# Kernel tuning notes

Hardware: AMD Instinct MI355X
Metric: run time of the kernel (lower is better)

The kernel has to match this reference:

```python
import jax, jax.numpy as jnp
import numpy as np

IN_DIM, HID, MEM, OUT = 512, 1024, 1024, 512
BATCH = 4096
HIST = 5  # hist_steps hard-coded in MMU.__init__

_LINEARS = [("inpgate", IN_DIM, HID), ("rec_inpgate", OUT, HID), ("mem_inpgate", MEM, HID),
            ("inp", IN_DIM, HID), ("rec_inp", OUT, HID),
            ("readgate", IN_DIM, MEM), ("rec_readgate", OUT, MEM), ("mem_readgate", MEM, MEM),
            ("decoder", HID, MEM),
            ("writegate", IN_DIM, MEM), ("rec_writegate", OUT, MEM), ("mem_writegate", MEM, MEM),
            ("encoder", MEM, HID)]


def setup_inputs() -> dict:
    key = jax.random.key(0)
    ks = iter(jax.random.split(key, 2 * len(_LINEARS) + 4))
    d = {"input": jax.random.normal(next(ks), (IN_DIM, BATCH), jnp.float32)}
    for name, fin, fout in _LINEARS:
        bound = 1.0 / np.sqrt(fin)  # torch nn.Linear default init range
        d["W_" + name] = jax.random.uniform(next(ks), (fout, fin), jnp.float32, -bound, bound)
        d["b_" + name] = jax.random.uniform(next(ks), (fout,), jnp.float32, -bound, bound)
    d["w_hid_out"] = jax.random.uniform(next(ks), (OUT, MEM), jnp.float32)  # torch.rand
    return d


def reference(input, W_inpgate, b_inpgate, W_rec_inpgate, b_rec_inpgate,
              W_mem_inpgate, b_mem_inpgate, W_inp, b_inp, W_rec_inp, b_rec_inp,
              W_readgate, b_readgate, W_rec_readgate, b_rec_readgate,
              W_mem_readgate, b_mem_readgate, W_decoder, b_decoder,
              W_writegate, b_writegate, W_rec_writegate, b_rec_writegate,
              W_mem_writegate, b_mem_writegate, W_encoder, b_encoder, w_hid_out):
    B = input.shape[1]
    lin = lambda x, W, b: x @ W.T + b
    # fresh module: history is zeros except last slot = current input (transposed to [B, in])
    xs = jnp.concatenate([jnp.zeros((HIST - 1, B, IN_DIM), input.dtype), input.T[None]], axis=0)

    def step(carry, x):
        out, mem = carry  # [B, OUT], [B, MEM]
        block_inp = jax.nn.sigmoid(lin(x, W_inp, b_inp) + lin(out, W_rec_inp, b_rec_inp))
        inp_gate = jax.nn.sigmoid(lin(x, W_inpgate, b_inpgate) + lin(mem, W_mem_inpgate, b_mem_inpgate)
                                  + lin(out, W_rec_inpgate, b_rec_inpgate))
        read_gate = jax.nn.sigmoid(lin(x, W_readgate, b_readgate) + lin(mem, W_mem_readgate, b_mem_readgate)
                                   + lin(out, W_rec_readgate, b_rec_readgate))
        decoded_mem = lin(read_gate * mem, W_decoder, b_decoder)
        hidden = decoded_mem + block_inp * inp_gate  # [B, HID] (HID == MEM)
        write_gate = jax.nn.sigmoid(lin(x, W_writegate, b_writegate) + lin(mem, W_mem_writegate, b_mem_writegate)
                                    + lin(out, W_rec_writegate, b_rec_writegate))
        encoded = jnp.tanh(lin(hidden, W_encoder, b_encoder))
        mem = (1.0 - write_gate) * mem + write_gate * encoded
        out = hidden @ w_hid_out.T  # w_hid_out.mm(hidden.T).T
        return (out, mem), None

    init = (jnp.zeros((B, OUT), input.dtype), jnp.zeros((B, MEM), input.dtype))
    (out, _mem), _ = jax.lax.scan(step, init, xs)
    return out
```

## Files before the change

kernel.cpp:

```cpp
#include <hip/hip_runtime.h>
#include <hip/hip_bf16.h>
#include <math.h>

typedef __hip_bfloat16 bf16;
typedef __attribute__((ext_vector_type(8))) short s16x8;
typedef __attribute__((ext_vector_type(4))) float f32x4;

__device__ __forceinline__ float fsig(float x) {
  return __builtin_amdgcn_rcpf(1.0f + __expf(-x));
}
__device__ __forceinline__ float ftanh(float x) { return 2.0f * fsig(2.0f * x) - 1.0f; }
__device__ __forceinline__ float dot4(float4 a, float4 b) {
  return a.x * b.x + a.y * b.y + a.z * b.z + a.w * b.w;
}

__global__ void setup(const float* __restrict__ W_inp, const float* __restrict__ W_ig,
                      const float* __restrict__ W_rg, const float* __restrict__ W_ho,
                      const float* __restrict__ W_dec, const float* __restrict__ input,
                      const float* __restrict__ b_inp, const float* __restrict__ b_rinp,
                      const float* __restrict__ b_ig, const float* __restrict__ b_mig,
                      const float* __restrict__ b_rig, const float* __restrict__ b_wg,
                      const float* __restrict__ b_mwg, const float* __restrict__ b_rwg,
                      const float* __restrict__ b_dec, bf16* __restrict__ Wcat,
                      bf16* __restrict__ WhoB, bf16* __restrict__ Wcat2, bf16* __restrict__ Wdt,
                      bf16* __restrict__ Xb, float* __restrict__ out_s, float* __restrict__ mem_s,
                      float* __restrict__ hidv, float* __restrict__ wgv,
                      float* __restrict__ vout) {
  __shared__ float t[32][33];
  const int id = blockIdx.x, tid = threadIdx.x;
  if (id < 8198) {
    const int i = id * 256 + tid;
    if (i < 524288) {
      Wcat[i] = __float2bfloat16(W_inp[i]);
    } else if (i < 1048576) {
      Wcat[i] = __float2bfloat16(W_ig[i - 524288]);
    } else if (i < 1572864) {
      Wcat[i] = __float2bfloat16(W_rg[i - 1048576]);
    } else if (i < 2097152) {
      const int k = i - 1572864;
      const bf16 vv = __float2bfloat16(W_ho[k]);
      WhoB[k] = vv;
      Wcat2[(size_t)(k >> 10) * 2048 + (k & 1023)] = vv;
    } else if (i < 2098688) {
      const int tt = i - 2097152;
      if (tt < 512) out_s[tt] = 0.0f;
      else mem_s[tt - 512] = 0.0f;
    }
  } else if (id < 10246) {
    const int b = id - 8198;
    const int i0 = (b >> 7) * 32, b0 = (b & 127) * 32;
    const int tx = tid & 31, ty = tid >> 5;
#pragma unroll
    for (int r = ty; r < 32; r += 8) t[r][tx] = input[(size_t)(i0 + r) * 4096 + b0 + tx];
    __syncthreads();
#pragma unroll
    for (int r = ty; r < 32; r += 8)
      Xb[(size_t)(b0 + r) * 512 + i0 + tx] = __float2bfloat16(t[tx][r]);
  } else if (id < 11270) {
    const int b = id - 10246;
    const int j0 = (b >> 5) * 32, k0 = (b & 31) * 32;
    const int tx = tid & 31, ty = tid >> 5;
#pragma unroll
    for (int r = ty; r < 32; r += 8) t[r][tx] = W_dec[(size_t)(j0 + r) * 1024 + k0 + tx];
    __syncthreads();
#pragma unroll
    for (int r = ty; r < 32; r += 8)
      Wdt[(size_t)(k0 + r) * 1024 + j0 + tx] = __float2bfloat16(t[tx][r]);
  } else if (id < 11274) {
    const int j = (id - 11270) * 256 + tid;
    const float bi = fsig(b_inp[j] + b_rinp[j]);
    const float ig = fsig(b_ig[j] + b_mig[j] + b_rig[j]);
    hidv[j] = b_dec[j] + bi * ig;
    wgv[j] = fsig(b_wg[j] + b_mwg[j] + b_rwg[j]);
  } else {
    const int o = id - 11274;
    const float4 a = *(const float4*)(W_ho + (size_t)o * 1024 + tid * 4);
    const float4 b = *(const float4*)(b_dec + tid * 4);
    float s = dot4(a, b);
#pragma unroll
    for (int off = 32; off > 0; off >>= 1) s += __shfl_down(s, off, 64);
    if ((tid & 63) == 0) t[0][tid >> 6] = s;
    __syncthreads();
    if (tid == 0) vout[o] = t[0][0] + t[0][1] + t[0][2] + t[0][3];
  }
}

__global__ void step_gates(const float* __restrict__ Wri, const float* __restrict__ Wmig,
                           const float* __restrict__ Wrig, const float* __restrict__ Wmrg,
                           const float* __restrict__ Wrrg, const float* __restrict__ Wmwg,
                           const float* __restrict__ Wrwg, const float* __restrict__ b_inp,
                           const float* __restrict__ b_rinp, const float* __restrict__ b_ig,
                           const float* __restrict__ b_mig, const float* __restrict__ b_rig,
                           const float* __restrict__ b_rg, const float* __restrict__ b_mrg,
                           const float* __restrict__ b_rrg, const float* __restrict__ b_wg,
                           const float* __restrict__ b_mwg, const float* __restrict__ b_rwg,
                           const float* __restrict__ out_s, const float* __restrict__ mem_s,
                           float* __restrict__ rgm, float* __restrict__ h0v,
                           float* __restrict__ wgv) {
  __shared__ float red[7][4];
  const int j = blockIdx.x, tid = threadIdx.x, lane = tid & 63, wave = tid >> 6;
  const float4 z = make_float4(0.f, 0.f, 0.f, 0.f);
  const float4 o4 = (tid < 128) ? *(const float4*)(out_s + tid * 4) : z;
  const float4 m4 = *(const float4*)(mem_s + tid * 4);
  float p[7];
  p[0] = dot4((tid < 128) ? *(const float4*)(Wri + (size_t)j * 512 + tid * 4) : z, o4);
  p[1] = dot4(*(const float4*)(Wmig + (size_t)j * 1024 + tid * 4), m4);
  p[2] = dot4((tid < 128) ? *(const float4*)(Wrig + (size_t)j * 512 + tid * 4) : z, o4);
  p[3] = dot4(*(const float4*)(Wmrg + (size_t)j * 1024 + tid * 4), m4);
  p[4] = dot4((tid < 128) ? *(const float4*)(Wrrg + (size_t)j * 512 + tid * 4) : z, o4);
  p[5] = dot4(*(const float4*)(Wmwg + (size_t)j * 1024 + tid * 4), m4);
  p[6] = dot4((tid < 128) ? *(const float4*)(Wrwg + (size_t)j * 512 + tid * 4) : z, o4);
#pragma unroll
  for (int d = 0; d < 7; ++d) {
    float s = p[d];
#pragma unroll
    for (int off = 32; off > 0; off >>= 1) s += __shfl_down(s, off, 64);
    if (lane == 0) red[d][wave] = s;
  }
  __syncthreads();
  if (tid == 0) {
    float D[7];
#pragma unroll
    for (int d = 0; d < 7; ++d) D[d] = red[d][0] + red[d][1] + red[d][2] + red[d][3];
    const float abi = b_inp[j] + b_rinp[j] + D[0];
    const float aig = b_ig[j] + b_mig[j] + b_rig[j] + D[1] + D[2];
    const float arg = b_rg[j] + b_mrg[j] + b_rrg[j] + D[3] + D[4];
    const float awg = b_wg[j] + b_mwg[j] + b_rwg[j] + D[5] + D[6];
    rgm[j] = fsig(arg) * mem_s[j];
    h0v[j] = fsig(abi) * fsig(aig);
    wgv[j] = fsig(awg);
  }
}

__global__ void step_decode(const float* __restrict__ Wdec, const float* __restrict__ b_dec,
                            const float* __restrict__ rgm, const float* __restrict__ h0v,
                            float* __restrict__ hidv) {
  __shared__ float red[4];
  const int j = blockIdx.x, tid = threadIdx.x;
  const float4 a = *(const float4*)(Wdec + (size_t)j * 1024 + tid * 4);
  const float4 b = *(const float4*)(rgm + tid * 4);
  float s = dot4(a, b);
#pragma unroll
  for (int off = 32; off > 0; off >>= 1) s += __shfl_down(s, off, 64);
  if ((tid & 63) == 0) red[tid >> 6] = s;
  __syncthreads();
  if (tid == 0) hidv[j] = b_dec[j] + red[0] + red[1] + red[2] + red[3] + h0v[j];
}

__global__ void step_update(const float* __restrict__ Wenc, const float* __restrict__ b_enc,
                            const float* __restrict__ Who, const float* __restrict__ hidv,
                            const float* __restrict__ wgv, float* __restrict__ mem_s,
                            float* __restrict__ out_s) {
  __shared__ float red[4];
  const int id = blockIdx.x, tid = threadIdx.x;
  const float* row = (id < 1024) ? (Wenc + (size_t)id * 1024) : (Who + (size_t)(id - 1024) * 1024);
  const float4 a = *(const float4*)(row + tid * 4);
  const float4 b = *(const float4*)(hidv + tid * 4);
  float s = dot4(a, b);
#pragma unroll
  for (int off = 32; off > 0; off >>= 1) s += __shfl_down(s, off, 64);
  if ((tid & 63) == 0) red[tid >> 6] = s;
  __syncthreads();
  if (tid == 0) {
    const float d = red[0] + red[1] + red[2] + red[3];
    if (id < 1024) {
      const float wg = wgv[id];
      mem_s[id] = (1.0f - wg) * mem_s[id] + wg * ftanh(b_enc[id] + d);
    } else {
      out_s[id - 1024] = d;
    }
  }
}

__global__ __launch_bounds__(256) void update0_p(
    const float* __restrict__ Wenc, const float* __restrict__ b_enc,
    const float* __restrict__ Who, const float* __restrict__ hidv,
    const float* __restrict__ wgv, float* __restrict__ mem_s, float* __restrict__ out_s,
    const bf16* __restrict__ WhoB, const bf16* __restrict__ Wdt, float* __restrict__ P) {
  __shared__ char smem[16384];
  const int tid = threadIdx.x;
  if (blockIdx.x < 1536) {
    float* red = (float*)smem;
    const int id = blockIdx.x;
    const float* row =
        (id < 1024) ? (Wenc + (size_t)id * 1024) : (Who + (size_t)(id - 1024) * 1024);
    const float4 a = *(const float4*)(row + tid * 4);
    const float4 b = *(const float4*)(hidv + tid * 4);
    float s = dot4(a, b);
#pragma unroll
    for (int off = 32; off > 0; off >>= 1) s += __shfl_down(s, off, 64);
    if ((tid & 63) == 0) red[tid >> 6] = s;
    __syncthreads();
    if (tid == 0) {
      const float d = red[0] + red[1] + red[2] + red[3];
      if (id < 1024) {
        const float wg = wgv[id];
        mem_s[id] = (1.0f - wg) * mem_s[id] + wg * ftanh(b_enc[id] + d);
      } else {
        out_s[id - 1024] = d;
      }
    }
    return;
  }
  const int bi = blockIdx.x - 1536;
  const int wave = tid >> 6, lane = tid & 63;
  const int wm = wave >> 1, wn = wave & 1;
  const int m0 = ((bi >> 4) & 7) * 64, n0 = (bi & 15) * 64;
  const int kt0 = (bi >> 7) * 512;
  f32x4 acc[2][2] = {};
  for (int kt = kt0; kt < kt0 + 512; kt += 64) {
    __syncthreads();
#pragma unroll
    for (int i = 0; i < 2; ++i) {
      const int ci = i * 256 + tid;
      const int row = ci >> 3, ck = (ci & 7) ^ (row & 7);
      const bf16* g = WhoB + (size_t)(m0 + row) * 1024 + kt + ck * 8;
      const unsigned lofs = (unsigned)__builtin_amdgcn_readfirstlane((i * 256 + wave * 64) * 16);
      __builtin_amdgcn_global_load_lds(
          (const __attribute__((address_space(1))) void*)g,
          (__attribute__((address_space(3))) void*)(smem + lofs), 16, 0, 0);
    }
#pragma unroll
    for (int i = 0; i < 2; ++i) {
      const int ci = i * 256 + tid;
      const int row = ci >> 3, ck = (ci & 7) ^ (row & 7);
      const bf16* g = Wdt + (size_t)(n0 + row) * 1024 + kt + ck * 8;
      const unsigned lofs =
          (unsigned)__builtin_amdgcn_readfirstlane(8192 + (i * 256 + wave * 64) * 16);
      __builtin_amdgcn_global_load_lds(
          (const __attribute__((address_space(1))) void*)g,
          (__attribute__((address_space(3))) void*)(smem + lofs), 16, 0, 0);
    }
    __syncthreads();
#pragma unroll
    for (int ks = 0; ks < 2; ++ks) {
      const int ckk = ks * 4 + (lane >> 4);
      s16x8 af[2];
#pragma unroll
      for (int i = 0; i < 2; ++i) {
        const int R = wm * 32 + i * 16 + (lane & 15);
        af[i] = *(const s16x8*)(smem + (R * 8 + (ckk ^ (R & 7))) * 16);
      }
#pragma unroll
      for (int j = 0; j < 2; ++j) {
        const int R = wn * 32 + j * 16 + (lane & 15);
        const s16x8 bfr = *(const s16x8*)(smem + 8192 + (R * 8 + (ckk ^ (R & 7))) * 16);
#pragma unroll
        for (int i = 0; i < 2; ++i)
          acc[i][j] = __builtin_amdgcn_mfma_f32_16x16x32_bf16(af[i], bfr, acc[i][j], 0, 0, 0);
      }
    }
  }
  const int mb = (lane >> 4) * 4, nb = lane & 15;
#pragma unroll
  for (int i = 0; i < 2; ++i) {
#pragma unroll
    for (int j = 0; j < 2; ++j) {
      const int col = n0 + wn * 32 + j * 16 + nb;
#pragma unroll
      for (int r = 0; r < 4; ++r) {
        const int rowg = m0 + wm * 32 + i * 16 + mb + r;
        atomicAdd(P + (size_t)rowg * 1024 + col, acc[i][j][r]);
      }
    }
  }
}

__global__ void final_consts(const float* __restrict__ Wri, const float* __restrict__ Wmig,
                             const float* __restrict__ Wrig, const float* __restrict__ Wmrg,
                             const float* __restrict__ Wrrg, const float* __restrict__ b_inp,
                             const float* __restrict__ b_rinp, const float* __restrict__ b_ig,
                             const float* __restrict__ b_mig, const float* __restrict__ b_rig,
                             const float* __restrict__ b_rg, const float* __restrict__ b_mrg,
                             const float* __restrict__ b_rrg, const float* __restrict__ out_s,
                             const float* __restrict__ mem_s, const float* __restrict__ P,
                             float* __restrict__ ccat, bf16* __restrict__ Wcat2) {
  __shared__ float red[5][4];
  const int id = blockIdx.x, tid = threadIdx.x, lane = tid & 63, wave = tid >> 6;
  if (id < 1024) {
    const float4 z = make_float4(0.f, 0.f, 0.f, 0.f);
    const float4 o4 = (tid < 128) ? *(const float4*)(out_s + tid * 4) : z;
    const float4 m4 = *(const float4*)(mem_s + tid * 4);
    float p[5];
    p[0] = dot4((tid < 128) ? *(const float4*)(Wri + (size_t)id * 512 + tid * 4) : z, o4);
    p[1] = dot4(*(const float4*)(Wmig + (size_t)id * 1024 + tid * 4), m4);
    p[2] = dot4((tid < 128) ? *(const float4*)(Wrig + (size_t)id * 512 + tid * 4) : z, o4);
    p[3] = dot4(*(const float4*)(Wmrg + (size_t)id * 1024 + tid * 4), m4);
    p[4] = dot4((tid < 128) ? *(const float4*)(Wrrg + (size_t)id * 512 + tid * 4) : z, o4);
#pragma unroll
    for (int d = 0; d < 5; ++d) {
      float s = p[d];
#pragma unroll
      for (int off = 32; off > 0; off >>= 1) s += __shfl_down(s, off, 64);
      if (lane == 0) red[d][wave] = s;
    }
    __syncthreads();
    if (tid == 0) {
      float D[5];
#pragma unroll
      for (int d = 0; d < 5; ++d) D[d] = red[d][0] + red[d][1] + red[d][2] + red[d][3];
      ccat[id] = b_inp[id] + b_rinp[id] + D[0];
      ccat[1024 + id] = b_ig[id] + b_mig[id] + b_rig[id] + D[1] + D[2];
      ccat[2048 + id] = b_rg[id] + b_mrg[id] + b_rrg[id] + D[3] + D[4];
    }
  } else {
    const int idx = (id - 1024) * 256 + tid;
    const int q = idx >> 10, k = idx & 1023;
    Wcat2[(size_t)q * 2048 + 1024 + k] = __float2bfloat16(P[idx] * mem_s[k]);
  }
}

__global__ __launch_bounds__(256, 4) void gemm_gates(const bf16* __restrict__ A,
                                                     const bf16* __restrict__ Wcat,
                                                     const float* __restrict__ ccat,
                                                     bf16* __restrict__ Hcat) {
  __shared__ char smem[32768];
  const int tid = threadIdx.x, wave = tid >> 6, lane = tid & 63;
  const int wm = wave >> 1, wn = wave & 1;
  const int m0 = blockIdx.y * 64, n0 = blockIdx.x * 64;
  f32x4 acc[3][2][2] = {};

  for (int kt = 0; kt < 512; kt += 64) {
    __syncthreads();
#pragma unroll
    for (int i = 0; i < 2; ++i) {
      const int ci = i * 256 + tid;
      const int row = ci >> 3, ck = (ci & 7) ^ (row & 7);
      const bf16* g = A + (size_t)(m0 + row) * 512 + kt + ck * 8;
      const unsigned lofs = (unsigned)__builtin_amdgcn_readfirstlane((i * 256 + wave * 64) * 16);
      __builtin_amdgcn_global_load_lds(
          (const __attribute__((address_space(1))) void*)g,
          (__attribute__((address_space(3))) void*)(smem + lofs), 16, 0, 0);
    }
#pragma unroll
    for (int gI = 0; gI < 3; ++gI) {
      const bf16* Bp = Wcat + gI * 524288;
#pragma unroll
      for (int i = 0; i < 2; ++i) {
        const int ci = i * 256 + tid;
        const int row = ci >> 3, ck = (ci & 7) ^ (row & 7);
        const bf16* g = Bp + (size_t)(n0 + row) * 512 + kt + ck * 8;
        const unsigned lofs = (unsigned)__builtin_amdgcn_readfirstlane(
            8192 + gI * 8192 + (i * 256 + wave * 64) * 16);
        __builtin_amdgcn_global_load_lds(
            (const __attribute__((address_space(1))) void*)g,
            (__attribute__((address_space(3))) void*)(smem + lofs), 16, 0, 0);
      }
    }
    __syncthreads();

#pragma unroll
    for (int ks = 0; ks < 2; ++ks) {
      const int ckk = ks * 4 + (lane >> 4);
      s16x8 af[2];
#pragma unroll
      for (int i = 0; i < 2; ++i) {
        const int R = wm * 32 + i * 16 + (lane & 15);
        af[i] = *(const s16x8*)(smem + (R * 8 + (ckk ^ (R & 7))) * 16);
      }
#pragma unroll
      for (int gI = 0; gI < 3; ++gI) {
#pragma unroll
        for (int j = 0; j < 2; ++j) {
          const int R = wn * 32 + j * 16 + (lane & 15);
          const s16x8 bfr =
              *(const s16x8*)(smem + 8192 + gI * 8192 + (R * 8 + (ckk ^ (R & 7))) * 16);
#pragma unroll
          for (int i = 0; i < 2; ++i)
            acc[gI][i][j] =
                __builtin_amdgcn_mfma_f32_16x16x32_bf16(af[i], bfr, acc[gI][i][j], 0, 0, 0);
        }
      }
    }
  }

  __syncthreads();
  bf16* sm = (bf16*)smem;
  bf16* sr = (bf16*)smem + 5120;
  const int mb = (lane >> 4) * 4, nb = lane & 15;
#pragma unroll
  for (int i = 0; i < 2; ++i) {
#pragma unroll
    for (int j = 0; j < 2; ++j) {
      const int colL = wn * 32 + j * 16 + nb;
      const int jg = n0 + colL;
      const float c0 = ccat[jg], c1 = ccat[1024 + jg], c2 = ccat[2048 + jg];
#pragma unroll
      for (int r = 0; r < 4; ++r) {
        const int rowL = wm * 32 + i * 16 + mb + r;
        const float h = fsig(acc[0][i][j][r] + c0) * fsig(acc[1][i][j][r] + c1);
        const float rg = fsig(acc[2][i][j][r] + c2);
        sm[rowL * 80 + colL] = __float2bfloat16(h);
        sr[rowL * 80 + colL] = __float2bfloat16(rg);
      }
    }
  }
  __syncthreads();
#pragma unroll
  for (int pp = 0; pp < 2; ++pp) {
    const int c = pp * 256 + tid;
    const int row = c >> 3, cc = c & 7;
    const s16x8 v0 = *(const s16x8*)(sm + row * 80 + cc * 8);
    const s16x8 v1 = *(const s16x8*)(sr + row * 80 + cc * 8);
    *(s16x8*)(Hcat + (size_t)(m0 + row) * 2048 + n0 + cc * 8) = v0;
    *(s16x8*)(Hcat + (size_t)(m0 + row) * 2048 + 1024 + n0 + cc * 8) = v1;
  }
}

__global__ __launch_bounds__(256, 4) void gemm_out(const bf16* __restrict__ A,
                                                   const bf16* __restrict__ Bp,
                                                   const float* __restrict__ vout,
                                                   float* __restrict__ outF) {
  __shared__ char smem[16384];
  const int tid = threadIdx.x, wave = tid >> 6, lane = tid & 63;
  const int wm = wave >> 1, wn = wave & 1;
  const int m0 = blockIdx.y * 64, n0 = blockIdx.x * 64;
  f32x4 acc[2][2] = {};

  for (int kt = 0; kt < 2048; kt += 64) {
    __syncthreads();
#pragma unroll
    for (int i = 0; i < 2; ++i) {
      const int ci = i * 256 + tid;
      const int row = ci >> 3, ck = (ci & 7) ^ (row & 7);
      const bf16* g = A + (size_t)(m0 + row) * 2048 + kt + ck * 8;
      const unsigned lofs = (unsigned)__builtin_amdgcn_readfirstlane((i * 256 + wave * 64) * 16);
      __builtin_amdgcn_global_load_lds(
          (const __attribute__((address_space(1))) void*)g,
          (__attribute__((address_space(3))) void*)(smem + lofs), 16, 0, 0);
    }
#pragma unroll
    for (int i = 0; i < 2; ++i) {
      const int ci = i * 256 + tid;
      const int row = ci >> 3, ck = (ci & 7) ^ (row & 7);
      const bf16* g = Bp + (size_t)(n0 + row) * 2048 + kt + ck * 8;
      const unsigned lofs =
          (unsigned)__builtin_amdgcn_readfirstlane(8192 + (i * 256 + wave * 64) * 16);
      __builtin_amdgcn_global_load_lds(
          (const __attribute__((address_space(1))) void*)g,
          (__attribute__((address_space(3))) void*)(smem + lofs), 16, 0, 0);
    }
    __syncthreads();

#pragma unroll
    for (int ks = 0; ks < 2; ++ks) {
      const int ckk = ks * 4 + (lane >> 4);
      s16x8 af[2];
#pragma unroll
      for (int i = 0; i < 2; ++i) {
        const int R = wm * 32 + i * 16 + (lane & 15);
        af[i] = *(const s16x8*)(smem + (R * 8 + (ckk ^ (R & 7))) * 16);
      }
#pragma unroll
      for (int j = 0; j < 2; ++j) {
        const int R = wn * 32 + j * 16 + (lane & 15);
        const s16x8 bfr = *(const s16x8*)(smem + 8192 + (R * 8 + (ckk ^ (R & 7))) * 16);
#pragma unroll
        for (int i = 0; i < 2; ++i)
          acc[i][j] = __builtin_amdgcn_mfma_f32_16x16x32_bf16(af[i], bfr, acc[i][j], 0, 0, 0);
      }
    }
  }

  const int mb = (lane >> 4) * 4, nb = lane & 15;
#pragma unroll
  for (int i = 0; i < 2; ++i) {
#pragma unroll
    for (int j = 0; j < 2; ++j) {
      const int col = n0 + wn * 32 + j * 16 + nb;
#pragma unroll
      for (int r = 0; r < 4; ++r) {
        const int rowg = m0 + wm * 32 + i * 16 + mb + r;
        outF[(size_t)rowg * 512 + col] = acc[i][j][r] + vout[col];
      }
    }
  }
}

extern "C" void kernel_launch(void* const* d_in, const int* in_sizes, int n_in, void* d_out,
                              int out_size, void* d_ws, size_t ws_size, hipStream_t stream) {
  const float* input  = (const float*)d_in[0];
  const float* W_ig   = (const float*)d_in[1];  const float* b_ig   = (const float*)d_in[2];
  const float* W_rig  = (const float*)d_in[3];  const float* b_rig  = (const float*)d_in[4];
  const float* W_mig  = (const float*)d_in[5];  const float* b_mig  = (const float*)d_in[6];
  const float* W_inp  = (const float*)d_in[7];  const float* b_inp  = (const float*)d_in[8];
  const float* W_rinp = (const float*)d_in[9];  const float* b_rinp = (const float*)d_in[10];
  const float* W_rg   = (const float*)d_in[11]; const float* b_rg   = (const float*)d_in[12];
  const float* W_rrg  = (const float*)d_in[13]; const float* b_rrg  = (const float*)d_in[14];
  const float* W_mrg  = (const float*)d_in[15]; const float* b_mrg  = (const float*)d_in[16];
  const float* W_dec  = (const float*)d_in[17]; const float* b_dec  = (const float*)d_in[18];
  const float* W_wg   = (const float*)d_in[19]; const float* b_wg   = (const float*)d_in[20];
  const float* W_rwg  = (const float*)d_in[21]; const float* b_rwg  = (const float*)d_in[22];
  const float* W_mwg  = (const float*)d_in[23]; const float* b_mwg  = (const float*)d_in[24];
  const float* W_enc  = (const float*)d_in[25]; const float* b_enc  = (const float*)d_in[26];
  const float* W_ho   = (const float*)d_in[27];
  (void)W_wg; (void)W_rwg; (void)W_mwg;

  char* ws = (char*)d_ws;
  float* out_s = (float*)(ws + 0);
  float* mem_s = (float*)(ws + 4096);
  float* rgm   = (float*)(ws + 8192);
  float* h0v   = (float*)(ws + 12288);
  float* wgv   = (float*)(ws + 16384);
  float* hidv  = (float*)(ws + 20480);
  float* ccat  = (float*)(ws + 24576);
  float* vout  = (float*)(ws + 40960);
  float* P     = (float*)(ws + 65536);
  bf16* Xb     = (bf16*)(ws + 2162688);
  bf16* Wcat   = (bf16*)(ws + 6356992);
  bf16* WhoB   = (bf16*)(ws + 9502720);
  bf16* Wcat2  = (bf16*)(ws + 10551296);
  bf16* Wdt    = (bf16*)(ws + 12648448);
  bf16* Hcat   = (bf16*)(ws + 14745600);

  setup<<<11786, 256, 0, stream>>>(W_inp, W_ig, W_rg, W_ho, W_dec, input, b_inp, b_rinp, b_ig,
                                   b_mig, b_rig, b_wg, b_mwg, b_rwg, b_dec, Wcat, WhoB, Wcat2,
                                   Wdt, Xb, out_s, mem_s, hidv, wgv, vout);

  update0_p<<<1792, 256, 0, stream>>>(W_enc, b_enc, W_ho, hidv, wgv, mem_s, out_s, WhoB, Wdt, P);

  for (int s = 0; s < 3; ++s) {
    step_gates<<<1024, 256, 0, stream>>>(W_rinp, W_mig, W_rig, W_mrg, W_rrg, W_mwg, W_rwg, b_inp,
                                         b_rinp, b_ig, b_mig, b_rig, b_rg, b_mrg, b_rrg, b_wg,
                                         b_mwg, b_rwg, out_s, mem_s, rgm, h0v, wgv);
    step_decode<<<1024, 256, 0, stream>>>(W_dec, b_dec, rgm, h0v, hidv);
    step_update<<<1536, 256, 0, stream>>>(W_enc, b_enc, W_ho, hidv, wgv, mem_s, out_s);
  }

  final_consts<<<3072, 256, 0, stream>>>(W_rinp, W_mig, W_rig, W_mrg, W_rrg, b_inp, b_rinp, b_ig,
                                         b_mig, b_rig, b_rg, b_mrg, b_rrg, out_s, mem_s, P, ccat,
                                         Wcat2);

  gemm_gates<<<dim3(16, 64), 256, 0, stream>>>(Xb, Wcat, ccat, Hcat);

  gemm_out<<<dim3(8, 64), 256, 0, stream>>>(Hcat, Wcat2, vout, (float*)d_out);
}
```

Before: 227.7 us.

## Fold decoder into encoder via precomputed W_enc·W_dec product, drop decode kernel

Precomputes E = W_enc·W_dec (bf16 MFMA, split-K atomics) and venc = W_enc·b_dec, so each recurrent step computes the encoder and output projections directly from h0 and read_gate*mem. This removes the step_decode launch and its dependent pass over W_dec in each of the three steps. In exchange, setup does more conversion work, a 1024x1024 GEMM is added up front, and E is held at bf16-derived precision, which may shift numerics slightly.

```diff
diff --git a/kernel.cpp b/kernel.cpp
--- a/kernel.cpp
+++ b/kernel.cpp
@@ -16,16 +16,18 @@
 
 __global__ void setup(const float* __restrict__ W_inp, const float* __restrict__ W_ig,
                       const float* __restrict__ W_rg, const float* __restrict__ W_ho,
-                      const float* __restrict__ W_dec, const float* __restrict__ input,
+                      const float* __restrict__ W_dec, const float* __restrict__ W_enc,
+                      const float* __restrict__ input,
                       const float* __restrict__ b_inp, const float* __restrict__ b_rinp,
                       const float* __restrict__ b_ig, const float* __restrict__ b_mig,
                       const float* __restrict__ b_rig, const float* __restrict__ b_wg,
                       const float* __restrict__ b_mwg, const float* __restrict__ b_rwg,
                       const float* __restrict__ b_dec, bf16* __restrict__ Wcat,
                       bf16* __restrict__ WhoB, bf16* __restrict__ Wcat2, bf16* __restrict__ Wdt,
-                      bf16* __restrict__ Xb, float* __restrict__ out_s, float* __restrict__ mem_s,
+                      bf16* __restrict__ WencB, bf16* __restrict__ Xb,
+                      float* __restrict__ out_s, float* __restrict__ mem_s,
                       float* __restrict__ hidv, float* __restrict__ wgv,
-                      float* __restrict__ vout) {
+                      float* __restrict__ vout, float* __restrict__ venc) {
   __shared__ float t[32][33];
   const int id = blockIdx.x, tid = threadIdx.x;
   if (id < 8198) {
@@ -72,16 +74,128 @@
     const float ig = fsig(b_ig[j] + b_mig[j] + b_rig[j]);
     hidv[j] = b_dec[j] + bi * ig;
     wgv[j] = fsig(b_wg[j] + b_mwg[j] + b_rwg[j]);
-  } else {
-    const int o = id - 11274;
-    const float4 a = *(const float4*)(W_ho + (size_t)o * 1024 + tid * 4);
+  } else if (id < 12810) {
+    const int isv = (id < 11786);
+    const int o = isv ? (id - 11274) : (id - 11786);
+    const float* row = isv ? (W_ho + (size_t)o * 1024) : (W_enc + (size_t)o * 1024);
+    const float4 a = *(const float4*)(row + tid * 4);
     const float4 b = *(const float4*)(b_dec + tid * 4);
     float s = dot4(a, b);
 #pragma unroll
     for (int off = 32; off > 0; off >>= 1) s += __shfl_down(s, off, 64);
     if ((tid & 63) == 0) t[0][tid >> 6] = s;
     __syncthreads();
-    if (tid == 0) vout[o] = t[0][0] + t[0][1] + t[0][2] + t[0][3];
+    if (tid == 0) {
+      const float v = t[0][0] + t[0][1] + t[0][2] + t[0][3];
+      if (isv) vout[o] = v; else venc[o] = v;
+    }
+  } else {
+    const int i = (id - 12810) * 256 + tid;
+    WencB[i] = __float2bfloat16(W_enc[i]);
+  }
+}
+
+__global__ __launch_bounds__(256) void update0_pe(
+    const float* __restrict__ Wenc, const float* __restrict__ b_enc,
+    const float* __restrict__ Who, const float* __restrict__ hidv,
+    const float* __restrict__ wgv, float* __restrict__ mem_s, float* __restrict__ out_s,
+    const bf16* __restrict__ WhoB, const bf16* __restrict__ WencB,
+    const bf16* __restrict__ Wdt, float* __restrict__ P, float* __restrict__ E) {
+  __shared__ char smem[16384];
+  const int tid = threadIdx.x;
+  if (blockIdx.x < 1536) {
+    float* red = (float*)smem;
+    const int id = blockIdx.x;
+    const float* row =
+        (id < 1024) ? (Wenc + (size_t)id * 1024) : (Who + (size_t)(id - 1024) * 1024);
+    const float4 a = *(const float4*)(row + tid * 4);
+    const float4 b = *(const float4*)(hidv + tid * 4);
+    float s = dot4(a, b);
+#pragma unroll
+    for (int off = 32; off > 0; off >>= 1) s += __shfl_down(s, off, 64);
+    if ((tid & 63) == 0) red[tid >> 6] = s;
+    __syncthreads();
+    if (tid == 0) {
+      const float d = red[0] + red[1] + red[2] + red[3];
+      if (id < 1024) {
+        const float wg = wgv[id];
+        mem_s[id] = (1.0f - wg) * mem_s[id] + wg * ftanh(b_enc[id] + d);
+      } else {
+        out_s[id - 1024] = d;
+      }
+    }
+    return;
+  }
+  const int bi = blockIdx.x - 1536;
+  const bf16* Ap;
+  float* Cp;
+  int m0, n0, kt0;
+  if (bi < 256) {
+    Ap = WhoB; Cp = P;
+    m0 = ((bi >> 4) & 7) * 64; n0 = (bi & 15) * 64; kt0 = (bi >> 7) * 512;
+  } else {
+    const int ei = bi - 256;
+    Ap = WencB; Cp = E;
+    m0 = ((ei >> 4) & 15) * 64; n0 = (ei & 15) * 64; kt0 = (ei >> 8) * 512;
+  }
+  const int wave = tid >> 6, lane = tid & 63;
+  const int wm = wave >> 1, wn = wave & 1;
+  f32x4 acc[2][2] = {};
+  for (int kt = kt0; kt < kt0 + 512; kt += 64) {
+    __syncthreads();
+#pragma unroll
+    for (int i = 0; i < 2; ++i) {
+      const int ci = i * 256 + tid;
+      const int row = ci >> 3, ck = (ci & 7) ^ (row & 7);
+      const bf16* g = Ap + (size_t)(m0 + row) * 1024 + kt + ck * 8;
+      const unsigned lofs = (unsigned)__builtin_amdgcn_readfirstlane((i * 256 + wave * 64) * 16);
+      __builtin_amdgcn_global_load_lds(
+          (const __attribute__((address_space(1))) void*)g,
+          (__attribute__((address_space(3))) void*)(smem + lofs), 16, 0, 0);
+    }
+#pragma unroll
+    for (int i = 0; i < 2; ++i) {
+      const int ci = i * 256 + tid;
+      const int row = ci >> 3, ck = (ci & 7) ^ (row & 7);
+      const bf16* g = Wdt + (size_t)(n0 + row) * 1024 + kt + ck * 8;
+      const unsigned lofs =
+          (unsigned)__builtin_amdgcn_readfirstlane(8192 + (i * 256 + wave * 64) * 16);
+      __builtin_amdgcn_global_load_lds(
+          (const __attribute__((address_space(1))) void*)g,
+          (__attribute__((address_space(3))) void*)(smem + lofs), 16, 0, 0);
+    }
+    __syncthreads();
+#pragma unroll
+    for (int ks = 0; ks < 2; ++ks) {
+      const int ckk = ks * 4 + (lane >> 4);
+      s16x8 af[2];
+#pragma unroll
+      for (int i = 0; i < 2; ++i) {
+        const int R = wm * 32 + i * 16 + (lane & 15);
+        af[i] = *(const s16x8*)(smem + (R * 8 + (ckk ^ (R & 7))) * 16);
+      }
+#pragma unroll
+      for (int j = 0; j < 2; ++j) {
+        const int R = wn * 32 + j * 16 + (lane & 15);
+        const s16x8 bfr = *(const s16x8*)(smem + 8192 + (R * 8 + (ckk ^ (R & 7))) * 16);
+#pragma unroll
+        for (int i = 0; i < 2; ++i)
+          acc[i][j] = __builtin_amdgcn_mfma_f32_16x16x32_bf16(af[i], bfr, acc[i][j], 0, 0, 0);
+      }
+    }
+  }
+  const int mb = (lane >> 4) * 4, nb = lane & 15;
+#pragma unroll
+  for (int i = 0; i < 2; ++i) {
+#pragma unroll
+    for (int j = 0; j < 2; ++j) {
+      const int col = n0 + wn * 32 + j * 16 + nb;
+#pragma unroll
+      for (int r = 0; r < 4; ++r) {
+        const int rowg = m0 + wm * 32 + i * 16 + mb + r;
+        atomicAdd(Cp + (size_t)rowg * 1024 + col, acc[i][j][r]);
+      }
+    }
   }
 }
 
@@ -132,136 +246,40 @@
   }
 }
 
-__global__ void step_decode(const float* __restrict__ Wdec, const float* __restrict__ b_dec,
-                            const float* __restrict__ rgm, const float* __restrict__ h0v,
-                            float* __restrict__ hidv) {
-  __shared__ float red[4];
-  const int j = blockIdx.x, tid = threadIdx.x;
-  const float4 a = *(const float4*)(Wdec + (size_t)j * 1024 + tid * 4);
-  const float4 b = *(const float4*)(rgm + tid * 4);
-  float s = dot4(a, b);
-#pragma unroll
-  for (int off = 32; off > 0; off >>= 1) s += __shfl_down(s, off, 64);
-  if ((tid & 63) == 0) red[tid >> 6] = s;
-  __syncthreads();
-  if (tid == 0) hidv[j] = b_dec[j] + red[0] + red[1] + red[2] + red[3] + h0v[j];
-}
-
-__global__ void step_update(const float* __restrict__ Wenc, const float* __restrict__ b_enc,
-                            const float* __restrict__ Who, const float* __restrict__ hidv,
-                            const float* __restrict__ wgv, float* __restrict__ mem_s,
-                            float* __restrict__ out_s) {
-  __shared__ float red[4];
-  const int id = blockIdx.x, tid = threadIdx.x;
-  const float* row = (id < 1024) ? (Wenc + (size_t)id * 1024) : (Who + (size_t)(id - 1024) * 1024);
-  const float4 a = *(const float4*)(row + tid * 4);
-  const float4 b = *(const float4*)(hidv + tid * 4);
-  float s = dot4(a, b);
-#pragma unroll
-  for (int off = 32; off > 0; off >>= 1) s += __shfl_down(s, off, 64);
-  if ((tid & 63) == 0) red[tid >> 6] = s;
+__global__ void step_update2(const float* __restrict__ Wenc, const float* __restrict__ b_enc,
+                             const float* __restrict__ venc, const float* __restrict__ E,
+                             const float* __restrict__ Who, const float* __restrict__ vout,
+                             const float* __restrict__ P, const float* __restrict__ h0v,
+                             const float* __restrict__ rgm, const float* __restrict__ wgv,
+                             float* __restrict__ mem_s, float* __restrict__ out_s) {
+  __shared__ float red[2][4];
+  const int id = blockIdx.x, tid = threadIdx.x, lane = tid & 63, wave = tid >> 6;
+  const float4 h4 = *(const float4*)(h0v + tid * 4);
+  const float4 r4 = *(const float4*)(rgm + tid * 4);
+  float s1, s2;
+  if (id < 1024) {
+    s1 = dot4(*(const float4*)(Wenc + (size_t)id * 1024 + tid * 4), h4);
+    s2 = dot4(*(const float4*)(E + (size_t)id * 1024 + tid * 4), r4);
+  } else {
+    const int o = id - 1024;
+    s1 = dot4(*(const float4*)(Who + (size_t)o * 1024 + tid * 4), h4);
+    s2 = dot4(*(const float4*)(P + (size_t)o * 1024 + tid * 4), r4);
+  }
+#pragma unroll
+  for (int off = 32; off > 0; off >>= 1) {
+    s1 += __shfl_down(s1, off, 64);
+    s2 += __shfl_down(s2, off, 64);
+  }
+  if (lane == 0) { red[0][wave] = s1; red[1][wave] = s2; }
   __syncthreads();
   if (tid == 0) {
-    const float d = red[0] + red[1] + red[2] + red[3];
+    const float D1 = red[0][0] + red[0][1] + red[0][2] + red[0][3];
+    const float D2 = red[1][0] + red[1][1] + red[1][2] + red[1][3];
     if (id < 1024) {
       const float wg = wgv[id];
-      mem_s[id] = (1.0f - wg) * mem_s[id] + wg * ftanh(b_enc[id] + d);
+      mem_s[id] = (1.0f - wg) * mem_s[id] + wg * ftanh(b_enc[id] + venc[id] + D1 + D2);
     } else {
-      out_s[id - 1024] = d;
-    }
-  }
-}
-
-__global__ __launch_bounds__(256) void update0_p(
-    const float* __restrict__ Wenc, const float* __restrict__ b_enc,
-    const float* __restrict__ Who, const float* __restrict__ hidv,
-    const float* __restrict__ wgv, float* __restrict__ mem_s, float* __restrict__ out_s,
-    const bf16* __restrict__ WhoB, const bf16* __restrict__ Wdt, float* __restrict__ P) {
-  __shared__ char smem[16384];
-  const int tid = threadIdx.x;
-  if (blockIdx.x < 1536) {
-    float* red = (float*)smem;
-    const int id = blockIdx.x;
-    const float* row =
-        (id < 1024) ? (Wenc + (size_t)id * 1024) : (Who + (size_t)(id - 1024) * 1024);
-    const float4 a = *(const float4*)(row + tid * 4);
-    const float4 b = *(const float4*)(hidv + tid * 4);
-    float s = dot4(a, b);
-#pragma unroll
-    for (int off = 32; off > 0; off >>= 1) s += __shfl_down(s, off, 64);
-    if ((tid & 63) == 0) red[tid >> 6] = s;
-    __syncthreads();
-    if (tid == 0) {
-      const float d = red[0] + red[1] + red[2] + red[3];
-      if (id < 1024) {
-        const float wg = wgv[id];
-        mem_s[id] = (1.0f - wg) * mem_s[id] + wg * ftanh(b_enc[id] + d);
-      } else {
-        out_s[id - 1024] = d;
-      }
-    }
-    return;
-  }
-  const int bi = blockIdx.x - 1536;
-  const int wave = tid >> 6, lane = tid & 63;
-  const int wm = wave >> 1, wn = wave & 1;
-  const int m0 = ((bi >> 4) & 7) * 64, n0 = (bi & 15) * 64;
-  const int kt0 = (bi >> 7) * 512;
-  f32x4 acc[2][2] = {};
-  for (int kt = kt0; kt < kt0 + 512; kt += 64) {
-    __syncthreads();
-#pragma unroll
-    for (int i = 0; i < 2; ++i) {
-      const int ci = i * 256 + tid;
-      const int row = ci >> 3, ck = (ci & 7) ^ (row & 7);
-      const bf16* g = WhoB + (size_t)(m0 + row) * 1024 + kt + ck * 8;
-      const unsigned lofs = (unsigned)__builtin_amdgcn_readfirstlane((i * 256 + wave * 64) * 16);
-      __builtin_amdgcn_global_load_lds(
-          (const __attribute__((address_space(1))) void*)g,
-          (__attribute__((address_space(3))) void*)(smem + lofs), 16, 0, 0);
-    }
-#pragma unroll
-    for (int i = 0; i < 2; ++i) {
-      const int ci = i * 256 + tid;
-      const int row = ci >> 3, ck = (ci & 7) ^ (row & 7);
-      const bf16* g = Wdt + (size_t)(n0 + row) * 1024 + kt + ck * 8;
-      const unsigned lofs =
-          (unsigned)__builtin_amdgcn_readfirstlane(8192 + (i * 256 + wave * 64) * 16);
-      __builtin_amdgcn_global_load_lds(
-          (const __attribute__((address_space(1))) void*)g,
-          (__attribute__((address_space(3))) void*)(smem + lofs), 16, 0, 0);
-    }
-    __syncthreads();
-#pragma unroll
-    for (int ks = 0; ks < 2; ++ks) {
-      const int ckk = ks * 4 + (lane >> 4);
-      s16x8 af[2];
-#pragma unroll
-      for (int i = 0; i < 2; ++i) {
-        const int R = wm * 32 + i * 16 + (lane & 15);
-        af[i] = *(const s16x8*)(smem + (R * 8 + (ckk ^ (R & 7))) * 16);
-      }
-#pragma unroll
-      for (int j = 0; j < 2; ++j) {
-        const int R = wn * 32 + j * 16 + (lane & 15);
-        const s16x8 bfr = *(const s16x8*)(smem + 8192 + (R * 8 + (ckk ^ (R & 7))) * 16);
-#pragma unroll
-        for (int i = 0; i < 2; ++i)
-          acc[i][j] = __builtin_amdgcn_mfma_f32_16x16x32_bf16(af[i], bfr, acc[i][j], 0, 0, 0);
-      }
-    }
-  }
-  const int mb = (lane >> 4) * 4, nb = lane & 15;
-#pragma unroll
-  for (int i = 0; i < 2; ++i) {
-#pragma unroll
-    for (int j = 0; j < 2; ++j) {
-      const int col = n0 + wn * 32 + j * 16 + nb;
-#pragma unroll
-      for (int r = 0; r < 4; ++r) {
-        const int rowg = m0 + wm * 32 + i * 16 + mb + r;
-        atomicAdd(P + (size_t)rowg * 1024 + col, acc[i][j][r]);
-      }
+      out_s[id - 1024] = vout[id - 1024] + D1 + D2;
     }
   }
 }
@@ -505,6 +523,7 @@
   float* hidv  = (float*)(ws + 20480);
   float* ccat  = (float*)(ws + 24576);
   float* vout  = (float*)(ws + 40960);
+  float* venc  = (float*)(ws + 45056);
   float* P     = (float*)(ws + 65536);
   bf16* Xb     = (bf16*)(ws + 2162688);
   bf16* Wcat   = (bf16*)(ws + 6356992);
@@ -512,19 +531,22 @@
   bf16* Wcat2  = (bf16*)(ws + 10551296);
   bf16* Wdt    = (bf16*)(ws + 12648448);
   bf16* Hcat   = (bf16*)(ws + 14745600);
-
-  setup<<<11786, 256, 0, stream>>>(W_inp, W_ig, W_rg, W_ho, W_dec, input, b_inp, b_rinp, b_ig,
-                                   b_mig, b_rig, b_wg, b_mwg, b_rwg, b_dec, Wcat, WhoB, Wcat2,
-                                   Wdt, Xb, out_s, mem_s, hidv, wgv, vout);
-
-  update0_p<<<1792, 256, 0, stream>>>(W_enc, b_enc, W_ho, hidv, wgv, mem_s, out_s, WhoB, Wdt, P);
+  float* E     = (float*)(ws + 31522816);
+  bf16* WencB  = (bf16*)(ws + 35717120);
+
+  setup<<<16906, 256, 0, stream>>>(W_inp, W_ig, W_rg, W_ho, W_dec, W_enc, input, b_inp, b_rinp,
+                                   b_ig, b_mig, b_rig, b_wg, b_mwg, b_rwg, b_dec, Wcat, WhoB,
+                                   Wcat2, Wdt, WencB, Xb, out_s, mem_s, hidv, wgv, vout, venc);
+
+  update0_pe<<<2304, 256, 0, stream>>>(W_enc, b_enc, W_ho, hidv, wgv, mem_s, out_s, WhoB, WencB,
+                                       Wdt, P, E);
 
   for (int s = 0; s < 3; ++s) {
     step_gates<<<1024, 256, 0, stream>>>(W_rinp, W_mig, W_rig, W_mrg, W_rrg, W_mwg, W_rwg, b_inp,
                                          b_rinp, b_ig, b_mig, b_rig, b_rg, b_mrg, b_rrg, b_wg,
                                          b_mwg, b_rwg, out_s, mem_s, rgm, h0v, wgv);
-    step_decode<<<1024, 256, 0, stream>>>(W_dec, b_dec, rgm, h0v, hidv);
-    step_update<<<1536, 256, 0, stream>>>(W_enc, b_enc, W_ho, hidv, wgv, mem_s, out_s);
+    step_update2<<<1536, 256, 0, stream>>>(W_enc, b_enc, venc, E, W_ho, vout, P, h0v, rgm, wgv,
+                                           mem_s, out_s);
   }
 
   final_consts<<<3072, 256, 0, stream>>>(W_rinp, W_mig, W_rig, W_mrg, W_rrg, b_inp, b_rinp, b_ig,
```

Result: slower. 232.9 us (+2.3%).
